# Optimization experiments

Measured on AMD Instinct MI355X. Metric: run time of the kernel, lower is better.

Reference implementation:

```python
import jax, jax.numpy as jnp
import numpy as np

DIM = 512      # input feature dim
REDUC = 64     # reduced dim
SR = 10        # sampling_rate
LOCAL = 20     # local_size
EPS = 1e-5     # torch LayerNorm default eps


def layer_norm(x, gamma, beta):
    mu = jnp.mean(x, axis=-1, keepdims=True)
    var = jnp.mean((x - mu) ** 2, axis=-1, keepdims=True)
    return (x - mu) / jnp.sqrt(var + EPS) * gamma + beta


def setup_inputs() -> dict:
    key = jax.random.key(0)
    ks = jax.random.split(key, 5)
    B, T = 32, 4096
    obs_frames = jax.random.normal(ks[0], (B, T, DIM), jnp.float32)
    s1 = 1.0 / np.sqrt(DIM)
    s2 = 1.0 / np.sqrt(REDUC)
    W1 = jax.random.uniform(ks[1], (DIM, REDUC), jnp.float32, -s1, s1)
    b1 = jax.random.uniform(ks[2], (REDUC,), jnp.float32, -s1, s1)
    g1 = jnp.ones((REDUC,), jnp.float32)
    beta1 = jnp.zeros((REDUC,), jnp.float32)
    W2 = jax.random.uniform(ks[3], (REDUC, DIM), jnp.float32, -s2, s2)
    b2 = jax.random.uniform(ks[4], (DIM,), jnp.float32, -s2, s2)
    g2 = jnp.ones((DIM,), jnp.float32)
    beta2 = jnp.zeros((DIM,), jnp.float32)
    return {"obs_frames": obs_frames, "W1": W1, "b1": b1, "g1": g1, "beta1": beta1,
            "W2": W2, "b2": b2, "g2": g2, "beta2": beta2}


def reference(obs_frames, W1, b1, g1, beta1, W2, b2, g2, beta2):
    # linear_reduction: Linear -> ReLU -> LayerNorm, (B,T,DIM) -> (B,T,REDUC)
    comp = layer_norm(jax.nn.relu(obs_frames @ W1 + b1), g1, beta1)
    # past pooling (max_abs): strided subsample of all but the last LOCAL steps
    past_pooled = jnp.max(comp[:, :-LOCAL:SR, :], axis=1)          # (B, REDUC)
    # compare_past_present: running max over the last LOCAL steps seeded by past_pooled
    present = comp[:, -LOCAL:, :]                                   # (B, LOCAL, REDUC)
    cm = jax.lax.cummax(present, axis=1)                            # fused cummax scan
    global_reduc = jnp.maximum(cm, past_pooled[:, None, :])         # (B, LOCAL, REDUC)
    # _linear_expand: Linear -> ReLU -> LayerNorm, (B,LOCAL,REDUC) -> (B,LOCAL,DIM)
    global_max = layer_norm(jax.nn.relu(global_reduc @ W2 + b2), g2, beta2)
    # return_max_now_reduc=False -> module returns (global_max, None); we return global_max
    return global_max
```

## Files before the change

kernel.cpp:

```cpp
#include <hip/hip_runtime.h>
#include <math.h>

#define DIM    512
#define REDUC  64
#define T_FULL 4096
#define NB     32
#define SR     10
#define N_SAMP 408
#define N_LOC  20
#define N_ROWS 428
#define EPS    1e-5f

#define RPB   32
#define BPB   14
#define NPART 13

typedef short bf16x8 __attribute__((ext_vector_type(8)));
typedef float f32x4  __attribute__((ext_vector_type(4)));

union Frag { bf16x8 v; uint4 u; };

__device__ __forceinline__ unsigned bf16_rne(float f) {
    unsigned u = __float_as_uint(f);
    return (u + 0x7fffu + ((u >> 16) & 1u)) >> 16;
}
__device__ __forceinline__ unsigned pack2(float lo, float hi) {
    return bf16_rne(lo) | (bf16_rne(hi) << 16);
}

__global__ __launch_bounds__(256) void k0_pack(const float* __restrict__ W1,
                                               uint4* __restrict__ w1p) {
    const int sg = blockIdx.x;
    const int t  = threadIdx.x;
    const int tile = t >> 6, l = t & 63;
    const int k0 = 32 * sg + 8 * (l >> 4);
    const int j  = 16 * tile + (l & 15);
    float v[8];
#pragma unroll
    for (int f = 0; f < 8; ++f) v[f] = W1[(size_t)(k0 + f) * REDUC + j];
    uint4 o;
    o.x = pack2(v[0], v[1]); o.y = pack2(v[2], v[3]);
    o.z = pack2(v[4], v[5]); o.w = pack2(v[6], v[7]);
    w1p[sg * 256 + t] = o;
}

__global__ __launch_bounds__(256) void k1_rows(
        const float* __restrict__ obs, const uint4* __restrict__ w1p,
        const float* __restrict__ b1, const float* __restrict__ g1,
        const float* __restrict__ beta1,
        float* __restrict__ partials, float* __restrict__ present)
{
    __shared__ Frag  abuf[8][256];
    __shared__ float comp[RPB][66];
    __shared__ float pmax[4][REDUC];

    const int t   = threadIdx.x;
    const int l   = t & 63;
    const int w   = t >> 6;
    const int blk = blockIdx.x;
    const int b   = blockIdx.y;

    const int s2s  = t >> 7;
    const int mts  = (t >> 6) & 1;
    const int rloc = 16 * mts + (l & 15);
    int rr = blk * RPB + rloc;
    int rc = (rr < N_ROWS) ? rr : 0;
    int tt = (rc < N_SAMP) ? rc * SR : (T_FULL - N_LOC) + (rc - N_SAMP);
    const float* xptr = obs + ((size_t)b * T_FULL + tt) * DIM
                        + 32 * s2s + 8 * (l >> 4);

    float4 xa[8], xb[8];
#pragma unroll
    for (int c = 0; c < 8; ++c) {
        xa[c] = *(const float4*)(xptr + 64 * c);
        xb[c] = *(const float4*)(xptr + 64 * c + 4);
    }
#pragma unroll
    for (int c = 0; c < 8; ++c) {
        Frag fr;
        fr.u.x = pack2(xa[c].x, xa[c].y); fr.u.y = pack2(xa[c].z, xa[c].w);
        fr.u.z = pack2(xb[c].x, xb[c].y); fr.u.w = pack2(xb[c].z, xb[c].w);
        abuf[c][t] = fr;
    }
    __syncthreads();

    const int mt = w >> 1, nh = w & 1;
    f32x4 acc0 = {0.f, 0.f, 0.f, 0.f};
    f32x4 acc1 = {0.f, 0.f, 0.f, 0.f};
#pragma unroll
    for (int c = 0; c < 8; ++c) {
#pragma unroll
        for (int s2 = 0; s2 < 2; ++s2) {
            Frag A; A.u = abuf[c][(s2 * 2 + mt) * 64 + l].u;
            const int sg = c * 2 + s2;
            Frag B0, B1;
            B0.u = w1p[(sg * 4 + 2 * nh + 0) * 64 + l];
            B1.u = w1p[(sg * 4 + 2 * nh + 1) * 64 + l];
            acc0 = __builtin_amdgcn_mfma_f32_16x16x32_bf16(A.v, B0.v, acc0, 0, 0, 0);
            acc1 = __builtin_amdgcn_mfma_f32_16x16x32_bf16(A.v, B1.v, acc1, 0, 0, 0);
        }
    }

    const int crow = 16 * mt + 4 * (l >> 4);
    const int ccol = 32 * nh + (l & 15);
#pragma unroll
    for (int r = 0; r < 4; ++r) {
        comp[crow + r][ccol]      = acc0[r];
        comp[crow + r][ccol + 16] = acc1[r];
    }
    __syncthreads();

    const float g1v = g1[l], be1v = beta1[l], b1v = b1[l];
    float wmax = -INFINITY;
#pragma unroll
    for (int r8 = 0; r8 < 8; ++r8) {
        int rl  = w * 8 + r8;
        int rr2 = blk * RPB + rl;
        float y = fmaxf(comp[rl][l] + b1v, 0.f);
        float s = y;
#pragma unroll
        for (int off = 32; off >= 1; off >>= 1) s += __shfl_xor(s, off);
        float mu = s * (1.f / 64.f);
        float d  = y - mu;
        float v  = d * d;
#pragma unroll
        for (int off = 32; off >= 1; off >>= 1) v += __shfl_xor(v, off);
        float cres = d * rsqrtf(v * (1.f / 64.f) + EPS) * g1v + be1v;

        if (rr2 < N_SAMP) {
            wmax = fmaxf(wmax, cres);
        } else if (rr2 < N_ROWS) {
            present[((size_t)b * N_LOC + (rr2 - N_SAMP)) * REDUC + l] = cres;
        }
    }

    pmax[w][l] = wmax;
    __syncthreads();
    if (w == 0 && blk < NPART) {
        float m = fmaxf(fmaxf(pmax[0][l], pmax[1][l]),
                        fmaxf(pmax[2][l], pmax[3][l]));
        partials[((size_t)b * NPART + blk) * REDUC + l] = m;
    }
}

__global__ __launch_bounds__(512) void k2_out(
        const float* __restrict__ partials,
        const float* __restrict__ present,
        const float* __restrict__ W2, const float* __restrict__ b2,
        const float* __restrict__ g2, const float* __restrict__ beta2,
        float* __restrict__ out)
{
    __shared__ float msh[8][REDUC];
    __shared__ float gsh[REDUC];
    __shared__ float red[16];

    const int b   = blockIdx.x / N_LOC;
    const int t   = blockIdx.x % N_LOC;
    const int tid = threadIdx.x;
    const int j   = tid & 63;
    const int s8  = tid >> 6;

    float m = -INFINITY;
    for (int p = s8; p < NPART; p += 8)
        m = fmaxf(m, partials[((size_t)b * NPART + p) * REDUC + j]);
    for (int r = s8; r <= t; r += 8)
        m = fmaxf(m, present[((size_t)b * N_LOC + r) * REDUC + j]);
    msh[s8][j] = m;
    __syncthreads();
    if (tid < REDUC) {
        float mm = msh[0][tid];
#pragma unroll
        for (int ss = 1; ss < 8; ++ss) mm = fmaxf(mm, msh[ss][tid]);
        gsh[tid] = mm;
    }
    __syncthreads();

    float acc = b2[tid];
#pragma unroll 8
    for (int k = 0; k < REDUC; ++k)
        acc = fmaf(gsh[k], W2[k * DIM + tid], acc);
    float y = fmaxf(acc, 0.f);

    const int lane = tid & 63, wv = tid >> 6;
    float s = y;
#pragma unroll
    for (int off = 32; off >= 1; off >>= 1) s += __shfl_xor(s, off);
    if (lane == 0) red[wv] = s;
    __syncthreads();
    float tot = red[0] + red[1] + red[2] + red[3] +
                red[4] + red[5] + red[6] + red[7];
    float mu = tot * (1.f / 512.f);
    float d  = y - mu;

    float v = d * d;
#pragma unroll
    for (int off = 32; off >= 1; off >>= 1) v += __shfl_xor(v, off);
    if (lane == 0) red[8 + wv] = v;
    __syncthreads();
    float vtot = red[8] + red[9] + red[10] + red[11] +
                 red[12] + red[13] + red[14] + red[15];
    float var = vtot * (1.f / 512.f);

    out[((size_t)b * N_LOC + t) * DIM + tid] =
        d * rsqrtf(var + EPS) * g2[tid] + beta2[tid];
}

extern "C" void kernel_launch(void* const* d_in, const int* in_sizes, int n_in,
                              void* d_out, int out_size, void* d_ws, size_t ws_size,
                              hipStream_t stream) {
    const float* obs   = (const float*)d_in[0];
    const float* W1    = (const float*)d_in[1];
    const float* b1    = (const float*)d_in[2];
    const float* g1    = (const float*)d_in[3];
    const float* beta1 = (const float*)d_in[4];
    const float* W2    = (const float*)d_in[5];
    const float* b2    = (const float*)d_in[6];
    const float* g2    = (const float*)d_in[7];
    const float* beta2 = (const float*)d_in[8];
    float* out = (float*)d_out;

    uint4* w1p      = (uint4*)d_ws;
    float* partials = (float*)((char*)d_ws + 65536);
    float* present  = partials + (size_t)NB * NPART * REDUC;

    k0_pack<<<16, 256, 0, stream>>>(W1, w1p);
    dim3 g1d(BPB, NB);
    k1_rows<<<g1d, 256, 0, stream>>>(obs, w1p, b1, g1, beta1, partials, present);
    k2_out<<<NB * N_LOC, 512, 0, stream>>>(partials, present, W2, b2, g2, beta2, out);
}
```

Before: 27.64 us.

## Fuse W1 bf16 packing into row kernel via shared memory, drop pack launch

Removes the separate W1 packing kernel. Each row block now loads W1 from global memory, converts it to bf16 and stores the MFMA B fragments in shared memory, in two halves of the K dimension, with the A staging buffer also split in half. This saves a kernel launch and its serial dependency, and B fragments are read from LDS instead of global memory. The cost is that every one of the 448 blocks repeats the W1 conversion, which adds redundant global loads and an extra barrier.

```diff
diff --git a/kernel.cpp b/kernel.cpp
--- a/kernel.cpp
+++ b/kernel.cpp
@@ -28,35 +28,20 @@
     return bf16_rne(lo) | (bf16_rne(hi) << 16);
 }
 
-__global__ __launch_bounds__(256) void k0_pack(const float* __restrict__ W1,
-                                               uint4* __restrict__ w1p) {
-    const int sg = blockIdx.x;
-    const int t  = threadIdx.x;
-    const int tile = t >> 6, l = t & 63;
-    const int k0 = 32 * sg + 8 * (l >> 4);
-    const int j  = 16 * tile + (l & 15);
-    float v[8];
-#pragma unroll
-    for (int f = 0; f < 8; ++f) v[f] = W1[(size_t)(k0 + f) * REDUC + j];
-    uint4 o;
-    o.x = pack2(v[0], v[1]); o.y = pack2(v[2], v[3]);
-    o.z = pack2(v[4], v[5]); o.w = pack2(v[6], v[7]);
-    w1p[sg * 256 + t] = o;
-}
-
 __global__ __launch_bounds__(256) void k1_rows(
-        const float* __restrict__ obs, const uint4* __restrict__ w1p,
+        const float* __restrict__ obs, const float* __restrict__ W1,
         const float* __restrict__ b1, const float* __restrict__ g1,
         const float* __restrict__ beta1,
         float* __restrict__ partials, float* __restrict__ present)
 {
-    __shared__ Frag  abuf[8][256];
+    __shared__ Frag  w1h[8 * 4 * 64];
+    __shared__ Frag  abuf[4][256];
     __shared__ float comp[RPB][66];
     __shared__ float pmax[4][REDUC];
 
     const int t   = threadIdx.x;
     const int l   = t & 63;
-    const int w   = t >> 6;
+    const int w   = __builtin_amdgcn_readfirstlane((int)(t >> 6));
     const int blk = blockIdx.x;
     const int b   = blockIdx.y;
 
@@ -75,29 +60,58 @@
         xa[c] = *(const float4*)(xptr + 64 * c);
         xb[c] = *(const float4*)(xptr + 64 * c + 4);
     }
-#pragma unroll
-    for (int c = 0; c < 8; ++c) {
-        Frag fr;
-        fr.u.x = pack2(xa[c].x, xa[c].y); fr.u.y = pack2(xa[c].z, xa[c].w);
-        fr.u.z = pack2(xb[c].x, xb[c].y); fr.u.w = pack2(xb[c].z, xb[c].w);
-        abuf[c][t] = fr;
-    }
-    __syncthreads();
+
+    const int sgW  = t >> 4;
+    const int tlW  = (t & 15) >> 2;
+    const int aW   = t & 3;
 
     const int mt = w >> 1, nh = w & 1;
     f32x4 acc0 = {0.f, 0.f, 0.f, 0.f};
     f32x4 acc1 = {0.f, 0.f, 0.f, 0.f};
-#pragma unroll
-    for (int c = 0; c < 8; ++c) {
-#pragma unroll
-        for (int s2 = 0; s2 < 2; ++s2) {
-            Frag A; A.u = abuf[c][(s2 * 2 + mt) * 64 + l].u;
-            const int sg = c * 2 + s2;
-            Frag B0, B1;
-            B0.u = w1p[(sg * 4 + 2 * nh + 0) * 64 + l];
-            B1.u = w1p[(sg * 4 + 2 * nh + 1) * 64 + l];
-            acc0 = __builtin_amdgcn_mfma_f32_16x16x32_bf16(A.v, B0.v, acc0, 0, 0, 0);
-            acc1 = __builtin_amdgcn_mfma_f32_16x16x32_bf16(A.v, B1.v, acc1, 0, 0, 0);
+
+    for (int h = 0; h < 2; ++h) {
+        if (h) __syncthreads();
+#pragma unroll
+        for (int c4 = 0; c4 < 4; ++c4) {
+            const int c = 4 * h + c4;
+            Frag fr;
+            fr.u.x = pack2(xa[c].x, xa[c].y); fr.u.y = pack2(xa[c].z, xa[c].w);
+            fr.u.z = pack2(xb[c].x, xb[c].y); fr.u.w = pack2(xb[c].z, xb[c].w);
+            abuf[c4][t] = fr;
+        }
+        if ((sgW >> 3) == h) {
+            const int sgl = sgW & 7;
+#pragma unroll
+            for (int c = 0; c < 4; ++c) {
+                float4 vf[8];
+#pragma unroll
+                for (int f = 0; f < 8; ++f)
+                    vf[f] = *(const float4*)(W1 + (size_t)(32*sgW + 8*aW + f) * REDUC
+                                             + 16*tlW + 4*c);
+#pragma unroll
+                for (int j = 0; j < 4; ++j) {
+                    Frag fr;
+                    fr.u.x = pack2(((float*)&vf[0])[j], ((float*)&vf[1])[j]);
+                    fr.u.y = pack2(((float*)&vf[2])[j], ((float*)&vf[3])[j]);
+                    fr.u.z = pack2(((float*)&vf[4])[j], ((float*)&vf[5])[j]);
+                    fr.u.w = pack2(((float*)&vf[6])[j], ((float*)&vf[7])[j]);
+                    w1h[(sgl * 4 + tlW) * 64 + 16*aW + 4*c + j] = fr;
+                }
+            }
+        }
+        __syncthreads();
+#pragma unroll
+        for (int c4 = 0; c4 < 4; ++c4) {
+#pragma unroll
+            for (int s2 = 0; s2 < 2; ++s2) {
+                const int sgl = c4 * 2 + s2;
+                Frag A; A.u = abuf[c4][(s2 * 2 + mt) * 64 + l].u;
+                Frag B0, B1;
+                B0.u = w1h[(sgl * 4 + 2 * nh + 0) * 64 + l].u;
+                B1.u = w1h[(sgl * 4 + 2 * nh + 1) * 64 + l].u;
+                acc0 = __builtin_amdgcn_mfma_f32_16x16x32_bf16(A.v, B0.v, acc0, 0, 0, 0);
+                acc1 = __builtin_amdgcn_mfma_f32_16x16x32_bf16(A.v, B1.v, acc1, 0, 0, 0);
+            }
         }
     }
 
@@ -219,12 +233,10 @@
     const float* beta2 = (const float*)d_in[8];
     float* out = (float*)d_out;
 
-    uint4* w1p      = (uint4*)d_ws;
-    float* partials = (float*)((char*)d_ws + 65536);
+    float* partials = (float*)d_ws;
     float* present  = partials + (size_t)NB * NPART * REDUC;
 
-    k0_pack<<<16, 256, 0, stream>>>(W1, w1p);
     dim3 g1d(BPB, NB);
-    k1_rows<<<g1d, 256, 0, stream>>>(obs, w1p, b1, g1, beta1, partials, present);
+    k1_rows<<<g1d, 256, 0, stream>>>(obs, W1, b1, g1, beta1, partials, present);
     k2_out<<<NB * N_LOC, 512, 0, stream>>>(partials, present, W2, b2, g2, beta2, out);
 }
```

After: 30.72 us. 11.1% more time.

## Halve rows per block in k1 and compute all local steps per batch in k2

Applied to the files above, without the earlier changes.

k1 now processes 16 rows per block with one MFMA tile per wave (27 blocks per batch instead of 14), so more blocks are in flight during the gather of obs rows. k2 is restructured from one 512-thread block per (batch, step) to one 256-thread block per batch: it computes the running max once, then reuses each W2 load across all 20 steps with register accumulators. This cuts redundant W2 traffic and the repeated partial reductions, but k2 now runs only 32 blocks with heavy register use, which risks low occupancy.

```diff
diff --git a/kernel.cpp b/kernel.cpp
--- a/kernel.cpp
+++ b/kernel.cpp
@@ -11,9 +11,9 @@
 #define N_ROWS 428
 #define EPS    1e-5f
 
-#define RPB   32
-#define BPB   14
-#define NPART 13
+#define RPB   16
+#define BPB   27
+#define NPART 26
 
 typedef short bf16x8 __attribute__((ext_vector_type(8)));
 typedef float f32x4  __attribute__((ext_vector_type(4)));
@@ -50,71 +50,62 @@
         const float* __restrict__ beta1,
         float* __restrict__ partials, float* __restrict__ present)
 {
-    __shared__ Frag  abuf[8][256];
+    __shared__ Frag  abuf[8][128];
     __shared__ float comp[RPB][66];
     __shared__ float pmax[4][REDUC];
 
     const int t   = threadIdx.x;
     const int l   = t & 63;
-    const int w   = t >> 6;
+    const int w   = __builtin_amdgcn_readfirstlane((int)(t >> 6));
     const int blk = blockIdx.x;
     const int b   = blockIdx.y;
 
-    const int s2s  = t >> 7;
-    const int mts  = (t >> 6) & 1;
-    const int rloc = 16 * mts + (l & 15);
+    const int s2s = t >> 7;
+    const int cs  = (t >> 6) & 1;
+    const int rloc = l & 15;
     int rr = blk * RPB + rloc;
     int rc = (rr < N_ROWS) ? rr : 0;
     int tt = (rc < N_SAMP) ? rc * SR : (T_FULL - N_LOC) + (rc - N_SAMP);
     const float* xptr = obs + ((size_t)b * T_FULL + tt) * DIM
                         + 32 * s2s + 8 * (l >> 4);
 
-    float4 xa[8], xb[8];
+    float4 xa[4], xb[4];
+#pragma unroll
+    for (int i = 0; i < 4; ++i) {
+        const int c = 2 * i + cs;
+        xa[i] = *(const float4*)(xptr + 64 * c);
+        xb[i] = *(const float4*)(xptr + 64 * c + 4);
+    }
+#pragma unroll
+    for (int i = 0; i < 4; ++i) {
+        Frag fr;
+        fr.u.x = pack2(xa[i].x, xa[i].y); fr.u.y = pack2(xa[i].z, xa[i].w);
+        fr.u.z = pack2(xb[i].x, xb[i].y); fr.u.w = pack2(xb[i].z, xb[i].w);
+        abuf[2 * i + cs][s2s * 64 + l] = fr;
+    }
+    __syncthreads();
+
+    f32x4 acc = {0.f, 0.f, 0.f, 0.f};
 #pragma unroll
     for (int c = 0; c < 8; ++c) {
-        xa[c] = *(const float4*)(xptr + 64 * c);
-        xb[c] = *(const float4*)(xptr + 64 * c + 4);
-    }
-#pragma unroll
-    for (int c = 0; c < 8; ++c) {
-        Frag fr;
-        fr.u.x = pack2(xa[c].x, xa[c].y); fr.u.y = pack2(xa[c].z, xa[c].w);
-        fr.u.z = pack2(xb[c].x, xb[c].y); fr.u.w = pack2(xb[c].z, xb[c].w);
-        abuf[c][t] = fr;
-    }
-    __syncthreads();
-
-    const int mt = w >> 1, nh = w & 1;
-    f32x4 acc0 = {0.f, 0.f, 0.f, 0.f};
-    f32x4 acc1 = {0.f, 0.f, 0.f, 0.f};
-#pragma unroll
-    for (int c = 0; c < 8; ++c) {
 #pragma unroll
         for (int s2 = 0; s2 < 2; ++s2) {
-            Frag A; A.u = abuf[c][(s2 * 2 + mt) * 64 + l].u;
-            const int sg = c * 2 + s2;
-            Frag B0, B1;
-            B0.u = w1p[(sg * 4 + 2 * nh + 0) * 64 + l];
-            B1.u = w1p[(sg * 4 + 2 * nh + 1) * 64 + l];
-            acc0 = __builtin_amdgcn_mfma_f32_16x16x32_bf16(A.v, B0.v, acc0, 0, 0, 0);
-            acc1 = __builtin_amdgcn_mfma_f32_16x16x32_bf16(A.v, B1.v, acc1, 0, 0, 0);
-        }
-    }
-
-    const int crow = 16 * mt + 4 * (l >> 4);
-    const int ccol = 32 * nh + (l & 15);
-#pragma unroll
-    for (int r = 0; r < 4; ++r) {
-        comp[crow + r][ccol]      = acc0[r];
-        comp[crow + r][ccol + 16] = acc1[r];
-    }
+            const int sg = 2 * c + s2;
+            Frag A; A.u = abuf[c][s2 * 64 + l].u;
+            Frag B; B.u = w1p[(sg * 4 + w) * 64 + l];
+            acc = __builtin_amdgcn_mfma_f32_16x16x32_bf16(A.v, B.v, acc, 0, 0, 0);
+        }
+    }
+#pragma unroll
+    for (int r = 0; r < 4; ++r)
+        comp[4 * (l >> 4) + r][16 * w + (l & 15)] = acc[r];
     __syncthreads();
 
     const float g1v = g1[l], be1v = beta1[l], b1v = b1[l];
     float wmax = -INFINITY;
 #pragma unroll
-    for (int r8 = 0; r8 < 8; ++r8) {
-        int rl  = w * 8 + r8;
+    for (int r8 = 0; r8 < 4; ++r8) {
+        int rl  = 4 * w + r8;
         int rr2 = blk * RPB + rl;
         float y = fmaxf(comp[rl][l] + b1v, 0.f);
         float s = y;
@@ -143,66 +134,86 @@
     }
 }
 
-__global__ __launch_bounds__(512) void k2_out(
+__global__ __launch_bounds__(256) void k2_out(
         const float* __restrict__ partials,
         const float* __restrict__ present,
         const float* __restrict__ W2, const float* __restrict__ b2,
         const float* __restrict__ g2, const float* __restrict__ beta2,
         float* __restrict__ out)
 {
-    __shared__ float msh[8][REDUC];
-    __shared__ float gsh[REDUC];
-    __shared__ float red[16];
-
-    const int b   = blockIdx.x / N_LOC;
-    const int t   = blockIdx.x % N_LOC;
-    const int tid = threadIdx.x;
-    const int j   = tid & 63;
-    const int s8  = tid >> 6;
-
-    float m = -INFINITY;
-    for (int p = s8; p < NPART; p += 8)
-        m = fmaxf(m, partials[((size_t)b * NPART + p) * REDUC + j]);
-    for (int r = s8; r <= t; r += 8)
-        m = fmaxf(m, present[((size_t)b * N_LOC + r) * REDUC + j]);
-    msh[s8][j] = m;
-    __syncthreads();
-    if (tid < REDUC) {
-        float mm = msh[0][tid];
-#pragma unroll
-        for (int ss = 1; ss < 8; ++ss) mm = fmaxf(mm, msh[ss][tid]);
-        gsh[tid] = mm;
-    }
-    __syncthreads();
-
-    float acc = b2[tid];
-#pragma unroll 8
-    for (int k = 0; k < REDUC; ++k)
-        acc = fmaf(gsh[k], W2[k * DIM + tid], acc);
-    float y = fmaxf(acc, 0.f);
-
-    const int lane = tid & 63, wv = tid >> 6;
-    float s = y;
-#pragma unroll
-    for (int off = 32; off >= 1; off >>= 1) s += __shfl_xor(s, off);
-    if (lane == 0) red[wv] = s;
-    __syncthreads();
-    float tot = red[0] + red[1] + red[2] + red[3] +
-                red[4] + red[5] + red[6] + red[7];
-    float mu = tot * (1.f / 512.f);
-    float d  = y - mu;
-
-    float v = d * d;
-#pragma unroll
-    for (int off = 32; off >= 1; off >>= 1) v += __shfl_xor(v, off);
-    if (lane == 0) red[8 + wv] = v;
-    __syncthreads();
-    float vtot = red[8] + red[9] + red[10] + red[11] +
-                 red[12] + red[13] + red[14] + red[15];
-    float var = vtot * (1.f / 512.f);
-
-    out[((size_t)b * N_LOC + t) * DIM + tid] =
-        d * rsqrtf(var + EPS) * g2[tid] + beta2[tid];
+    __shared__ float gall[N_LOC][REDUC];
+    __shared__ float red[N_LOC][4];
+    __shared__ float redv[N_LOC][4];
+
+    const int b = blockIdx.x;
+    const int t = threadIdx.x;
+    const int l = t & 63;
+    const int wv = t >> 6;
+
+    if (t < REDUC) {
+        float m = -INFINITY;
+#pragma unroll
+        for (int p = 0; p < NPART; ++p)
+            m = fmaxf(m, partials[((size_t)b * NPART + p) * REDUC + t]);
+        for (int s = 0; s < N_LOC; ++s) {
+            m = fmaxf(m, present[((size_t)b * N_LOC + s) * REDUC + t]);
+            gall[s][t] = m;
+        }
+    }
+    __syncthreads();
+
+    const int j0 = t, j1 = t + 256;
+    float acc0[N_LOC], acc1[N_LOC];
+    {
+        const float b20 = b2[j0], b21 = b2[j1];
+#pragma unroll
+        for (int r = 0; r < N_LOC; ++r) { acc0[r] = b20; acc1[r] = b21; }
+    }
+    for (int k = 0; k < REDUC; ++k) {
+        float w0  = W2[(size_t)k * DIM + j0];
+        float w1v = W2[(size_t)k * DIM + j1];
+#pragma unroll
+        for (int r = 0; r < N_LOC; ++r) {
+            float gv = gall[r][k];
+            acc0[r] = fmaf(gv, w0,  acc0[r]);
+            acc1[r] = fmaf(gv, w1v, acc1[r]);
+        }
+    }
+
+#pragma unroll
+    for (int r = 0; r < N_LOC; ++r) {
+        acc0[r] = fmaxf(acc0[r], 0.f);
+        acc1[r] = fmaxf(acc1[r], 0.f);
+        float s = acc0[r] + acc1[r];
+#pragma unroll
+        for (int off = 32; off >= 1; off >>= 1) s += __shfl_xor(s, off);
+        if (l == 0) red[r][wv] = s;
+    }
+    __syncthreads();
+    float mu[N_LOC];
+#pragma unroll
+    for (int r = 0; r < N_LOC; ++r)
+        mu[r] = (red[r][0] + red[r][1] + red[r][2] + red[r][3]) * (1.f / 512.f);
+#pragma unroll
+    for (int r = 0; r < N_LOC; ++r) {
+        float d0 = acc0[r] - mu[r], d1 = acc1[r] - mu[r];
+        float v = d0 * d0 + d1 * d1;
+#pragma unroll
+        for (int off = 32; off >= 1; off >>= 1) v += __shfl_xor(v, off);
+        if (l == 0) redv[r][wv] = v;
+    }
+    __syncthreads();
+    {
+        const float g20 = g2[j0], g21 = g2[j1];
+        const float be20 = beta2[j0], be21 = beta2[j1];
+#pragma unroll
+        for (int r = 0; r < N_LOC; ++r) {
+            float var = (redv[r][0] + redv[r][1] + redv[r][2] + redv[r][3]) * (1.f / 512.f);
+            float inv = rsqrtf(var + EPS);
+            out[((size_t)b * N_LOC + r) * DIM + j0] = (acc0[r] - mu[r]) * inv * g20 + be20;
+            out[((size_t)b * N_LOC + r) * DIM + j1] = (acc1[r] - mu[r]) * inv * g21 + be21;
+        }
+    }
 }
 
 extern "C" void kernel_launch(void* const* d_in, const int* in_sizes, int n_in,
@@ -226,5 +237,5 @@
     k0_pack<<<16, 256, 0, stream>>>(W1, w1p);
     dim3 g1d(BPB, NB);
     k1_rows<<<g1d, 256, 0, stream>>>(obs, w1p, b1, g1, beta1, partials, present);
-    k2_out<<<NB * N_LOC, 512, 0, stream>>>(partials, present, W2, b2, g2, beta2, out);
-}
+    k2_out<<<NB, 256, 0, stream>>>(partials, present, W2, b2, g2, beta2, out);
+}
```

New measurement: 41.08 us. 48.6% more time.
